# Optimization experiments

Hardware: AMD Instinct MI355X
Metric: run time of the kernel (lower is better)

Reference implementation:

```python
import jax, jax.numpy as jnp
import numpy as np

N = 512      # state dim n
K = 8        # num_regimes
H = 256      # hidden dim for g0/g1/gate MLPs
B = 8192     # batch
INIT_SCALE = 0.1


def _mlp(x, w1, b1, w2, b2, w3, b3):
    # 2 hidden SiLU layers + linear head (matches ScalarMLP/GateNet with num_layers=2)
    h = jax.nn.silu(x @ w1 + b1)
    h = jax.nn.silu(h @ w2 + b2)
    return h @ w3 + b3


def setup_inputs() -> dict:
    key = jax.random.key(0)
    ks = jax.random.split(key, 12)

    def lin(k, fi, fo):
        kw, kb = jax.random.split(k)
        s = 1.0 / np.sqrt(fi)  # torch nn.Linear default init range
        w = jax.random.uniform(kw, (fi, fo), minval=-s, maxval=s, dtype=jnp.float32)
        b = jax.random.uniform(kb, (fo,), minval=-s, maxval=s, dtype=jnp.float32)
        return w, b

    g0_w1, g0_b1 = lin(ks[0], N, H)
    g0_w2, g0_b2 = lin(ks[1], H, H)
    g0_w3, g0_b3 = lin(ks[2], H, 1)
    g1_w1, g1_b1 = lin(ks[3], N, H)
    g1_w2, g1_b2 = lin(ks[4], H, H)
    g1_w3, g1_b3 = lin(ks[5], H, 1)
    gt_w1, gt_b1 = lin(ks[6], N, H)
    gt_w2, gt_b2 = lin(ks[7], H, H)
    gt_w3, gt_b3 = lin(ks[8], H, K)
    W = jax.random.uniform(ks[9], (K, N, N), minval=-INIT_SCALE, maxval=INIT_SCALE, dtype=jnp.float32)
    z = jax.random.normal(ks[10], (B, 2 * N), dtype=jnp.float32)
    return dict(z=z,
                g0_w1=g0_w1, g0_b1=g0_b1, g0_w2=g0_w2, g0_b2=g0_b2, g0_w3=g0_w3, g0_b3=g0_b3,
                g1_w1=g1_w1, g1_b1=g1_b1, g1_w2=g1_w2, g1_b2=g1_b2, g1_w3=g1_w3, g1_b3=g1_b3,
                gt_w1=gt_w1, gt_b1=gt_b1, gt_w2=gt_w2, gt_b2=gt_b2, gt_w3=gt_w3, gt_b3=gt_b3,
                W=W)


def reference(z,
              g0_w1, g0_b1, g0_w2, g0_b2, g0_w3, g0_b3,
              g1_w1, g1_b1, g1_w2, g1_b2, g1_w3, g1_b3,
              gt_w1, gt_b1, gt_w2, gt_b2, gt_w3, gt_b3,
              W):
    n = W.shape[-1]
    x0, x1 = z[:, :n], z[:, n:]

    def U(x0_, x1_):
        e0 = jnp.sum(_mlp(x0_, g0_w1, g0_b1, g0_w2, g0_b2, g0_w3, g0_b3))  # scalar
        e1 = jnp.sum(_mlp(x1_, g1_w1, g1_b1, g1_w2, g1_b2, g1_w3, g1_b3))
        alpha = jax.nn.softmax(_mlp(x0_, gt_w1, gt_b1, gt_w2, gt_b2, gt_w3, gt_b3), axis=-1)  # [B,K]
        # per-sample per-regime bilinear x1^T W_k x0 -> avoids materializing [B,n,n] W_eff
        q = jnp.einsum('bi,kij,bj->bk', x1_, W, x0_)
        return e0 + e1 + jnp.sum(alpha * q)

    grad_x0, grad_x1 = jax.grad(U, argnums=(0, 1))(x0, x1)
    return jnp.concatenate([-grad_x0, -grad_x1], axis=-1)  # [B, 2n]
```

## Files before the change

kernel.cpp:

```cpp
#include <hip/hip_runtime.h>
#include <cstdint>
#include <cstddef>

constexpr int BTOT = 8192, N = 512, H = 256, K = 8;

typedef __attribute__((ext_vector_type(8))) short short8v;
typedef __attribute__((ext_vector_type(4))) float f32x4;

__device__ __forceinline__ float bf2f(unsigned short u) {
    return __uint_as_float(((uint32_t)u) << 16);
}
__device__ __forceinline__ unsigned short f2bf(float f) {
    uint32_t u = __float_as_uint(f);
    uint32_t r = (u + 0x7FFFu + ((u >> 16) & 1u)) >> 16;
    return (unsigned short)r;
}

typedef __attribute__((address_space(3))) unsigned int lds_uint;
typedef __attribute__((address_space(1))) const unsigned int glob_uint;
__device__ __forceinline__ void async16(const unsigned short* g, unsigned short* l) {
    __builtin_amdgcn_global_load_lds((glob_uint*)g, (lds_uint*)l, 16, 0, 0);
}

struct GArg {
    const unsigned short* A;
    const unsigned short* Bt;
    const float* bias;
    const unsigned short* dmul;
    const float* alpha;
    const unsigned short* vsub;
    unsigned short* ob;
    unsigned short* ob2;
    float* of;
    int lda, ldbt, Ka, lddm, ldob, ldof;
};

enum { EPI_BF = 0, EPI_FWD = 1, EPI_BWD2 = 2, EPI_NEG = 3, EPI_NEGV = 4 };

template<int EPI>
__global__ __launch_bounds__(256) void gemm_g(GArg ga0, GArg ga1, GArg ga2)
{
    const int z = blockIdx.z;
    const GArg g = (z == 0) ? ga0 : (z == 1) ? ga1 : ga2;

    __shared__ __attribute__((aligned(16))) unsigned short As[2][128 * 32];
    __shared__ __attribute__((aligned(16))) unsigned short Bs[2][128 * 32];
    const int tid = threadIdx.x;
    const int lane = tid & 63, wave = tid >> 6;
    const int m0 = blockIdx.y * 128, n0 = blockIdx.x * 128;
    const int wr = (wave >> 1) * 64, wc = (wave & 1) * 64;
    const int rr = lane & 15;
    const int kb = ((lane >> 4) ^ (lane & 3)) << 3;

    const int r0 = tid >> 2;
    const int ko0 = (((tid & 3) ^ (r0 & 3)) << 3);
    const unsigned short* gA0 = g.A + (size_t)(m0 + r0) * g.lda + ko0;
    const unsigned short* gA1 = g.A + (size_t)(m0 + r0 + 64) * g.lda + ko0;
    const unsigned short* gB0 = g.Bt + (size_t)(n0 + r0) * g.ldbt + ko0;
    const unsigned short* gB1 = g.Bt + (size_t)(n0 + r0 + 64) * g.ldbt + ko0;

    f32x4 acc[4][4];
    #pragma unroll
    for (int i = 0; i < 4; ++i)
        #pragma unroll
        for (int j = 0; j < 4; ++j) acc[i][j] = (f32x4){0.f, 0.f, 0.f, 0.f};

    const int nt = g.Ka >> 5;

    async16(gA0, &As[0][tid * 8]);
    async16(gA1, &As[0][(tid + 256) * 8]);
    async16(gB0, &Bs[0][tid * 8]);
    async16(gB1, &Bs[0][(tid + 256) * 8]);
    asm volatile("s_waitcnt vmcnt(0)" ::: "memory");
    __builtin_amdgcn_s_barrier();

    int cur = 0;
    for (int t = 0; t < nt; ++t) {
        if (t + 1 < nt) {
            const int k0 = (t + 1) << 5;
            async16(gA0 + k0, &As[cur ^ 1][tid * 8]);
            async16(gA1 + k0, &As[cur ^ 1][(tid + 256) * 8]);
            async16(gB0 + k0, &Bs[cur ^ 1][tid * 8]);
            async16(gB1 + k0, &Bs[cur ^ 1][(tid + 256) * 8]);
        }
        short8v af[4], bfr[4];
        #pragma unroll
        for (int i = 0; i < 4; ++i)
            af[i] = *(const short8v*)(&As[cur][(wr + i * 16 + rr) * 32 + kb]);
        #pragma unroll
        for (int j = 0; j < 4; ++j)
            bfr[j] = *(const short8v*)(&Bs[cur][(wc + j * 16 + rr) * 32 + kb]);
        #pragma unroll
        for (int i = 0; i < 4; ++i)
            #pragma unroll
            for (int j = 0; j < 4; ++j)
                acc[i][j] = __builtin_amdgcn_mfma_f32_16x16x32_bf16(af[i], bfr[j], acc[i][j], 0, 0, 0);
        asm volatile("s_waitcnt vmcnt(0)" ::: "memory");
        __builtin_amdgcn_s_barrier();
        cur ^= 1;
    }

    const int orow = (lane >> 4) * 4;
    #pragma unroll
    for (int i = 0; i < 4; ++i) {
        #pragma unroll
        for (int e = 0; e < 4; ++e) {
            const int row = m0 + wr + i * 16 + orow + e;
            if constexpr (EPI == EPI_NEGV) {
                float al[K];
                #pragma unroll
                for (int kk = 0; kk < K; ++kk) al[kk] = g.alpha[(size_t)row * K + kk];
                #pragma unroll
                for (int j = 0; j < 4; ++j) {
                    const int col = n0 + wc + rr + j * 16;
                    const unsigned short* vp = g.vsub + (size_t)row * (K * N) + col;
                    float sub = 0.f;
                    #pragma unroll
                    for (int kk = 0; kk < K; ++kk) sub += al[kk] * bf2f(vp[(size_t)kk * N]);
                    g.of[(size_t)row * g.ldof + col] = -acc[i][j][e] - sub;
                }
            } else {
                #pragma unroll
                for (int j = 0; j < 4; ++j) {
                    const int col = n0 + wc + rr + j * 16;
                    float v = acc[i][j][e];
                    if constexpr (EPI == EPI_BF) {
                        g.ob[(size_t)row * g.ldob + col] = f2bf(v);
                    } else if constexpr (EPI == EPI_FWD) {
                        float p = v + g.bias[col];
                        float s = 1.f / (1.f + expf(-p));
                        if (g.ob) g.ob[(size_t)row * g.ldob + col] = f2bf(p * s);
                        g.ob2[(size_t)row * g.ldob + col] = f2bf(s * (1.f + p * (1.f - s)));
                    } else if constexpr (EPI == EPI_BWD2) {
                        float t = v * bf2f(g.dmul[(size_t)row * g.lddm + col]);
                        g.ob[(size_t)row * g.ldob + col] = f2bf(t);
                    } else if constexpr (EPI == EPI_NEG) {
                        g.of[(size_t)row * g.ldof + col] -= v;
                    }
                }
            }
        }
    }
}

__global__ __launch_bounds__(256) void k_cvt_z(const float* __restrict__ z,
                                               unsigned short* __restrict__ o) {
    int g = (blockIdx.x * 256 + threadIdx.x) * 4;
    float4 v = *(const float4*)(z + g);
    ushort4 u;
    u.x = f2bf(v.x); u.y = f2bf(v.y); u.z = f2bf(v.z); u.w = f2bf(v.w);
    *(ushort4*)(o + g) = u;
}

__global__ __launch_bounds__(256) void k_transpose_w(const float* __restrict__ W,
    unsigned short* __restrict__ Wbf, unsigned short* __restrict__ WTbf)
{
    __shared__ float t[32][33];
    int k = blockIdx.z;
    int i0 = blockIdx.y * 32, j0 = blockIdx.x * 32;
    int tj = threadIdx.x & 31, ti = threadIdx.x >> 5;
    const float* Wk = W + (size_t)k * N * N;
    #pragma unroll
    for (int r = 0; r < 32; r += 8) {
        float v = Wk[(size_t)(i0 + ti + r) * N + j0 + tj];
        t[ti + r][tj] = v;
        Wbf[(size_t)k * N * N + (size_t)(i0 + ti + r) * N + j0 + tj] = f2bf(v);
    }
    __syncthreads();
    #pragma unroll
    for (int r = 0; r < 32; r += 8)
        WTbf[(size_t)k * N * N + (size_t)(j0 + ti + r) * N + i0 + tj] = f2bf(t[tj][ti + r]);
}

struct CvtJob { const float* src; unsigned short* dst; int ls, ld, cols32, tiles, trans; };
struct CvtTable { CvtJob j[12]; };

__global__ __launch_bounds__(256) void k_cvt_w(CvtTable T)
{
    int t = blockIdx.x;
    int ji = 0;
    while (t >= T.j[ji].tiles) { t -= T.j[ji].tiles; ++ji; }
    CvtJob jb = T.j[ji];
    int i0 = (t / jb.cols32) * 32, c0 = (t % jb.cols32) * 32;
    int tc = threadIdx.x & 31, tr = threadIdx.x >> 5;
    if (!jb.trans) {
        #pragma unroll
        for (int r = 0; r < 32; r += 8)
            jb.dst[(size_t)(i0 + tr + r) * jb.ld + c0 + tc] =
                f2bf(jb.src[(size_t)(i0 + tr + r) * jb.ls + c0 + tc]);
    } else {
        __shared__ float tt[32][33];
        #pragma unroll
        for (int r = 0; r < 32; r += 8)
            tt[tr + r][tc] = jb.src[(size_t)(i0 + tr + r) * jb.ls + c0 + tc];
        __syncthreads();
        #pragma unroll
        for (int r = 0; r < 32; r += 8)
            jb.dst[(size_t)(c0 + tr + r) * jb.ld + i0 + tc] = f2bf(tt[tc][tr + r]);
    }
}

__global__ __launch_bounds__(256) void k_head_s(const unsigned short* __restrict__ h2t,
    const float* __restrict__ w3t, const float* __restrict__ b3t,
    float* __restrict__ s)
{
    int t = threadIdx.x;
    int bl = t >> 3, k = t & 7;
    int b = blockIdx.x * 32 + bl;
    const unsigned short* ar = h2t + (size_t)b * H;
    float acc = b3t[k];
    for (int h0 = 0; h0 < H; h0 += 8) {
        short8v hv = *(const short8v*)(ar + h0);
        #pragma unroll
        for (int u = 0; u < 8; ++u)
            acc += bf2f((unsigned short)hv[u]) * w3t[(h0 + u) * K + k];
    }
    s[b * K + k] = acc;
}

__global__ __launch_bounds__(256) void k_q(const unsigned short* __restrict__ v0,
    const unsigned short* __restrict__ zb, float* __restrict__ q)
{
    int w = threadIdx.x >> 6, lane = threadIdx.x & 63;
    int idx = blockIdx.x * 4 + w;
    int b = idx >> 3, k = idx & 7;
    const unsigned short* vr = v0 + ((size_t)b * K + k) * N;
    const unsigned short* xr = zb + (size_t)b * 1024 + 512;
    short8v vv = *(const short8v*)(vr + lane * 8);
    short8v xv = *(const short8v*)(xr + lane * 8);
    float s = 0.f;
    #pragma unroll
    for (int t = 0; t < 8; ++t)
        s += bf2f((unsigned short)vv[t]) * bf2f((unsigned short)xv[t]);
    for (int off = 32; off; off >>= 1) s += __shfl_down(s, off, 64);
    if (lane == 0) q[idx] = s;
}

__global__ __launch_bounds__(256) void k_d(const float* __restrict__ s,
    const float* __restrict__ q, float* __restrict__ alpha,
    float* __restrict__ dd, int Bc)
{
    int b = blockIdx.x * 256 + threadIdx.x;
    if (b >= Bc) return;
    float sv[K], qv[K];
    float m = -1e30f;
    #pragma unroll
    for (int k = 0; k < K; ++k) { sv[k] = s[b * K + k]; m = fmaxf(m, sv[k]); }
    float sum = 0.f;
    #pragma unroll
    for (int k = 0; k < K; ++k) { sv[k] = expf(sv[k] - m); sum += sv[k]; }
    float inv = 1.f / sum, qbar = 0.f;
    #pragma unroll
    for (int k = 0; k < K; ++k) { sv[k] *= inv; qv[k] = q[b * K + k]; qbar += sv[k] * qv[k]; }
    #pragma unroll
    for (int k = 0; k < K; ++k) {
        alpha[b * K + k] = sv[k];
        dd[b * K + k] = sv[k] * (qv[k] - qbar);
    }
}

__global__ __launch_bounds__(256) void k_u2(
    const unsigned short* __restrict__ d2_0, const unsigned short* __restrict__ d2_1,
    const unsigned short* __restrict__ d2_t,
    const float* __restrict__ w3_0, const float* __restrict__ w3_1,
    const float* __restrict__ w3t, const float* __restrict__ dd,
    unsigned short* __restrict__ u2_0, unsigned short* __restrict__ u2_1,
    unsigned short* __restrict__ u2_t)
{
    int g = blockIdx.x * 256 + threadIdx.x;
    int h = g & (H - 1), b = g >> 8;
    u2_0[g] = f2bf(w3_0[h] * bf2f(d2_0[g]));
    u2_1[g] = f2bf(w3_1[h] * bf2f(d2_1[g]));
    float s = 0.f;
    #pragma unroll
    for (int k = 0; k < K; ++k) s += w3t[h * K + k] * dd[b * K + k];
    u2_t[g] = f2bf(s * bf2f(d2_t[g]));
}

__global__ __launch_bounds__(256) void k_gxq2(const unsigned short* __restrict__ v0,
    const unsigned short* __restrict__ v1, const float* __restrict__ alpha,
    float* __restrict__ out)
{
    int g = blockIdx.x * 256 + threadIdx.x;
    int b = g >> 6, jb = (g & 63) << 3;
    float al[K];
    #pragma unroll
    for (int k = 0; k < K; ++k) al[k] = alpha[b * K + k];
    const unsigned short* pv0 = v0 + (size_t)b * K * N + jb;
    const unsigned short* pv1 = v1 + (size_t)b * K * N + jb;
    float s0[8] = {}, s1[8] = {};
    #pragma unroll
    for (int k = 0; k < K; ++k) {
        short8v w1 = *(const short8v*)(pv1 + (size_t)k * N);
        short8v w0 = *(const short8v*)(pv0 + (size_t)k * N);
        #pragma unroll
        for (int t = 0; t < 8; ++t) {
            s0[t] += al[k] * bf2f((unsigned short)w1[t]);
            s1[t] += al[k] * bf2f((unsigned short)w0[t]);
        }
    }
    float* o0 = out + (size_t)b * 1024 + jb;
    float* o1 = o0 + 512;
    float4 x0 = *(float4*)o0, x1 = *(float4*)(o0 + 4);
    x0.x -= s0[0]; x0.y -= s0[1]; x0.z -= s0[2]; x0.w -= s0[3];
    x1.x -= s0[4]; x1.y -= s0[5]; x1.z -= s0[6]; x1.w -= s0[7];
    *(float4*)o0 = x0; *(float4*)(o0 + 4) = x1;
    float4 y0 = *(float4*)o1, y1 = *(float4*)(o1 + 4);
    y0.x -= s1[0]; y0.y -= s1[1]; y0.z -= s1[2]; y0.w -= s1[3];
    y1.x -= s1[4]; y1.y -= s1[5]; y1.z -= s1[6]; y1.w -= s1[7];
    *(float4*)o1 = y0; *(float4*)(o1 + 4) = y1;
}

extern "C" void kernel_launch(void* const* d_in, const int* in_sizes, int n_in,
                              void* d_out, int out_size, void* d_ws, size_t ws_size,
                              hipStream_t stream) {
    const float* z     = (const float*)d_in[0];
    const float* g0_w1 = (const float*)d_in[1];  const float* g0_b1 = (const float*)d_in[2];
    const float* g0_w2 = (const float*)d_in[3];  const float* g0_b2 = (const float*)d_in[4];
    const float* g0_w3 = (const float*)d_in[5];
    const float* g1_w1 = (const float*)d_in[7];  const float* g1_b1 = (const float*)d_in[8];
    const float* g1_w2 = (const float*)d_in[9];  const float* g1_b2 = (const float*)d_in[10];
    const float* g1_w3 = (const float*)d_in[11];
    const float* gt_w1 = (const float*)d_in[13]; const float* gt_b1 = (const float*)d_in[14];
    const float* gt_w2 = (const float*)d_in[15]; const float* gt_b2 = (const float*)d_in[16];
    const float* gt_w3 = (const float*)d_in[17]; const float* gt_b3 = (const float*)d_in[18];
    const float* W     = (const float*)d_in[19];
    float* out = (float*)d_out;

    char* wsb = (char*)d_ws;
    size_t off = 0;
    auto aus = [&](size_t n) -> unsigned short* {
        unsigned short* r = (unsigned short*)(wsb + off);
        off += ((n * 2 + 255) & ~(size_t)255);
        return r;
    };
    auto af4 = [&](size_t n) -> float* {
        float* r = (float*)(wsb + off);
        off += ((n * 4 + 255) & ~(size_t)255);
        return r;
    };

    unsigned short* Zbf  = aus((size_t)BTOT * 1024);
    unsigned short* Wbf  = aus((size_t)K * N * N);
    unsigned short* WTbf = aus((size_t)K * N * N);
    unsigned short* w1T[3], *w2T[3], *w2N[3];
    for (int i = 0; i < 3; ++i) w1T[i] = aus((size_t)H * N);
    for (int i = 0; i < 3; ++i) w2T[i] = aus((size_t)H * H);
    for (int i = 0; i < 3; ++i) w2N[i] = aus((size_t)H * H);
    unsigned short* w1N1  = aus((size_t)N * H);
    unsigned short* w1cat = aus((size_t)N * 2 * H);
    unsigned short* h1[3], *d1b[3], *d2b[3], *u2[3];
    for (int i = 0; i < 3; ++i) h1[i]  = aus((size_t)BTOT * H);
    for (int i = 0; i < 3; ++i) d1b[i] = aus((size_t)BTOT * H);
    for (int i = 0; i < 3; ++i) d2b[i] = aus((size_t)BTOT * H);
    for (int i = 0; i < 3; ++i) u2[i]  = aus((size_t)BTOT * H);
    unsigned short* h2t   = aus((size_t)BTOT * H);
    unsigned short* t2cat = aus((size_t)BTOT * 512);
    unsigned short* t21   = aus((size_t)BTOT * H);
    float* sbuf = af4((size_t)BTOT * K);
    float* qbuf = af4((size_t)BTOT * K);
    float* abuf = af4((size_t)BTOT * K);
    float* dbuf = af4((size_t)BTOT * K);

    int Bcv = BTOT;
    while (off + 2 * (((size_t)Bcv * K * N * 2 + 255) & ~(size_t)255) > ws_size && Bcv > 128)
        Bcv >>= 1;
    unsigned short* v0 = aus((size_t)Bcv * K * N);
    unsigned short* v1 = aus((size_t)Bcv * K * N);
    const bool full = (Bcv == BTOT);

    const dim3 blk(256);

    if (!full)
        hipMemsetAsync(d_out, 0, (size_t)out_size * sizeof(float), stream);

    k_cvt_z<<<BTOT * 1024 / (256 * 4), blk, 0, stream>>>(z, Zbf);
    k_transpose_w<<<dim3(N / 32, N / 32, K), blk, 0, stream>>>(W, Wbf, WTbf);

    CvtTable T;
    int nj = 0, tot = 0;
    auto addjob = [&](const float* src, int ls, unsigned short* dst, int ld,
                      int rows, int cols, int trans) {
        CvtJob jb; jb.src = src; jb.dst = dst; jb.ls = ls; jb.ld = ld;
        jb.cols32 = cols / 32; jb.tiles = (rows / 32) * (cols / 32); jb.trans = trans;
        T.j[nj++] = jb; tot += jb.tiles;
    };
    addjob(g0_w1, H, w1T[0], N, N, H, 1);
    addjob(g1_w1, H, w1T[1], N, N, H, 1);
    addjob(gt_w1, H, w1T[2], N, N, H, 1);
    addjob(g0_w2, H, w2T[0], H, H, H, 1);
    addjob(g1_w2, H, w2T[1], H, H, H, 1);
    addjob(gt_w2, H, w2T[2], H, H, H, 1);
    addjob(g0_w2, H, w2N[0], H, H, H, 0);
    addjob(g1_w2, H, w2N[1], H, H, H, 0);
    addjob(gt_w2, H, w2N[2], H, H, H, 0);
    addjob(g1_w1, H, w1N1, H, N, H, 0);
    addjob(g0_w1, H, w1cat, 2 * H, N, H, 0);
    addjob(gt_w1, H, w1cat + H, 2 * H, N, H, 0);
    k_cvt_w<<<tot, blk, 0, stream>>>(T);

    auto mk = [](const unsigned short* A, int lda, const unsigned short* Bt, int ldbt, int Ka) {
        GArg g; g.A = A; g.Bt = Bt; g.bias = nullptr; g.dmul = nullptr;
        g.alpha = nullptr; g.vsub = nullptr;
        g.ob = nullptr; g.ob2 = nullptr; g.of = nullptr;
        g.lda = lda; g.ldbt = ldbt; g.Ka = Ka; g.lddm = 0; g.ldob = 0; g.ldof = 0;
        return g;
    };

    {
        const float* bs[3] = {g0_b1, g1_b1, gt_b1};
        GArg a[3];
        for (int i = 0; i < 3; ++i) {
            a[i] = mk(Zbf + (i == 1 ? 512 : 0), 1024, w1T[i], N, N);
            a[i].bias = bs[i]; a[i].ob = h1[i]; a[i].ob2 = d1b[i]; a[i].ldob = H;
        }
        gemm_g<EPI_FWD><<<dim3(H / 128, BTOT / 128, 3), blk, 0, stream>>>(a[0], a[1], a[2]);
    }
    {
        const float* bs[3] = {g0_b2, g1_b2, gt_b2};
        GArg a[3];
        for (int i = 0; i < 3; ++i) {
            a[i] = mk(h1[i], H, w2T[i], H, H);
            a[i].bias = bs[i]; a[i].ob = (i == 2) ? h2t : nullptr;
            a[i].ob2 = d2b[i]; a[i].ldob = H;
        }
        gemm_g<EPI_FWD><<<dim3(H / 128, BTOT / 128, 3), blk, 0, stream>>>(a[0], a[1], a[2]);
    }
    k_head_s<<<BTOT / 32, blk, 0, stream>>>(h2t, gt_w3, gt_b3, sbuf);

    for (int cb = 0; cb < BTOT; cb += Bcv) {
        GArg a[2];
        a[0] = mk(Zbf + (size_t)cb * 1024, 1024, Wbf, N, N);
        a[0].ob = v0; a[0].ldob = K * N;
        a[1] = mk(Zbf + (size_t)cb * 1024 + 512, 1024, WTbf, N, N);
        a[1].ob = v1; a[1].ldob = K * N;
        gemm_g<EPI_BF><<<dim3(K * N / 128, Bcv / 128, 2), blk, 0, stream>>>(a[0], a[1], a[1]);

        k_q<<<Bcv * K / 4, blk, 0, stream>>>(v0, Zbf + (size_t)cb * 1024, qbuf + (size_t)cb * K);
        k_d<<<(Bcv + 255) / 256, blk, 0, stream>>>(sbuf + (size_t)cb * K, qbuf + (size_t)cb * K,
                                                   abuf + (size_t)cb * K, dbuf + (size_t)cb * K, Bcv);
        if (!full)
            k_gxq2<<<Bcv * 64 / 256, blk, 0, stream>>>(v0, v1, abuf + (size_t)cb * K,
                                                       out + (size_t)cb * 1024);
    }

    k_u2<<<BTOT * H / 256, blk, 0, stream>>>(d2b[0], d2b[1], d2b[2],
                                             g0_w3, g1_w3, gt_w3, dbuf,
                                             u2[0], u2[1], u2[2]);

    {
        GArg a[3];
        a[0] = mk(u2[0], H, w2N[0], H, H);
        a[0].dmul = d1b[0]; a[0].lddm = H; a[0].ob = t2cat;     a[0].ldob = 512;
        a[1] = mk(u2[1], H, w2N[1], H, H);
        a[1].dmul = d1b[1]; a[1].lddm = H; a[1].ob = t21;       a[1].ldob = H;
        a[2] = mk(u2[2], H, w2N[2], H, H);
        a[2].dmul = d1b[2]; a[2].lddm = H; a[2].ob = t2cat + H; a[2].ldob = 512;
        gemm_g<EPI_BWD2><<<dim3(H / 128, BTOT / 128, 3), blk, 0, stream>>>(a[0], a[1], a[2]);
    }
    {
        GArg a[2];
        a[0] = mk(t2cat, 512, w1cat, 2 * H, 512);
        a[0].of = out;       a[0].ldof = 1024;
        a[1] = mk(t21, H, w1N1, H, H);
        a[1].of = out + 512; a[1].ldof = 1024;
        if (full) {
            a[0].alpha = abuf; a[0].vsub = v1;
            a[1].alpha = abuf; a[1].vsub = v0;
            gemm_g<EPI_NEGV><<<dim3(N / 128, BTOT / 128, 2), blk, 0, stream>>>(a[0], a[1], a[1]);
        } else {
            gemm_g<EPI_NEG><<<dim3(N / 128, BTOT / 128, 2), blk, 0, stream>>>(a[0], a[1], a[1]);
        }
    }
}
```

Before: 247.4 us.

## Fuse gate head and bilinear q reductions into GEMM epilogues via atomics

The gate head logits (h2·w3) are now reduced inside the second-layer forward GEMM epilogue, and q = x1·v0 inside the v0/v1 GEMM epilogue. Both use cross-lane shuffles plus atomicAdd into pre-zeroed buffers, which removes the k_head_s and k_q kernels and the h2t write and re-read. The gate bias is added later in k_d. A block-index swizzle over the N dimension is also added to change tile scheduling order. The costs are extra epilogue work, two memsets, atomic contention, and float atomics whose summation order is nondeterministic.

```diff
diff --git a/kernel.cpp b/kernel.cpp
--- a/kernel.cpp
+++ b/kernel.cpp
@@ -32,6 +32,10 @@
     unsigned short* ob;
     unsigned short* ob2;
     float* of;
+    float* qout;
+    const unsigned short* xq;
+    float* sout;
+    const float* w3s;
     int lda, ldbt, Ka, lddm, ldob, ldof;
 };
 
@@ -47,7 +51,11 @@
     __shared__ __attribute__((aligned(16))) unsigned short Bs[2][128 * 32];
     const int tid = threadIdx.x;
     const int lane = tid & 63, wave = tid >> 6;
-    const int m0 = blockIdx.y * 128, n0 = blockIdx.x * 128;
+
+    int bx = blockIdx.x;
+    if ((gridDim.x & 7) == 0) bx = (bx & 7) * (gridDim.x >> 3) + (bx >> 3);
+
+    const int m0 = blockIdx.y * 128, n0 = bx * 128;
     const int wr = (wave >> 1) * 64, wc = (wave & 1) * 64;
     const int rr = lane & 15;
     const int kb = ((lane >> 4) ^ (lane & 3)) << 3;
@@ -119,6 +127,38 @@
                     for (int kk = 0; kk < K; ++kk) sub += al[kk] * bf2f(vp[(size_t)kk * N]);
                     g.of[(size_t)row * g.ldof + col] = -acc[i][j][e] - sub;
                 }
+            } else if constexpr (EPI == EPI_FWD) {
+                float sq[K];
+                const bool do_s = (g.sout != nullptr);
+                #pragma unroll
+                for (int kk = 0; kk < K; ++kk) sq[kk] = 0.f;
+                #pragma unroll
+                for (int j = 0; j < 4; ++j) {
+                    const int col = n0 + wc + rr + j * 16;
+                    float p = acc[i][j][e] + g.bias[col];
+                    float s = 1.f / (1.f + expf(-p));
+                    if (g.ob) g.ob[(size_t)row * g.ldob + col] = f2bf(p * s);
+                    g.ob2[(size_t)row * g.ldob + col] = f2bf(s * (1.f + p * (1.f - s)));
+                    if (do_s) {
+                        float sl = p * s;
+                        float4 wa = *(const float4*)(g.w3s + (size_t)col * K);
+                        float4 wb = *(const float4*)(g.w3s + (size_t)col * K + 4);
+                        sq[0] += sl * wa.x; sq[1] += sl * wa.y;
+                        sq[2] += sl * wa.z; sq[3] += sl * wa.w;
+                        sq[4] += sl * wb.x; sq[5] += sl * wb.y;
+                        sq[6] += sl * wb.z; sq[7] += sl * wb.w;
+                    }
+                }
+                if (do_s) {
+                    #pragma unroll
+                    for (int m = 1; m < 16; m <<= 1)
+                        #pragma unroll
+                        for (int kk = 0; kk < K; ++kk) sq[kk] += __shfl_xor(sq[kk], m, 64);
+                    if ((lane & 15) == 0)
+                        #pragma unroll
+                        for (int kk = 0; kk < K; ++kk)
+                            atomicAdd(g.sout + (size_t)row * K + kk, sq[kk]);
+                }
             } else {
                 #pragma unroll
                 for (int j = 0; j < 4; ++j) {
@@ -126,11 +166,6 @@
                     float v = acc[i][j][e];
                     if constexpr (EPI == EPI_BF) {
                         g.ob[(size_t)row * g.ldob + col] = f2bf(v);
-                    } else if constexpr (EPI == EPI_FWD) {
-                        float p = v + g.bias[col];
-                        float s = 1.f / (1.f + expf(-p));
-                        if (g.ob) g.ob[(size_t)row * g.ldob + col] = f2bf(p * s);
-                        g.ob2[(size_t)row * g.ldob + col] = f2bf(s * (1.f + p * (1.f - s)));
                     } else if constexpr (EPI == EPI_BWD2) {
                         float t = v * bf2f(g.dmul[(size_t)row * g.lddm + col]);
                         g.ob[(size_t)row * g.ldob + col] = f2bf(t);
@@ -139,6 +174,21 @@
                     }
                 }
             }
+            if constexpr (EPI == EPI_BF) {
+                if (g.qout) {
+                    const int kq = n0 >> 9, i0 = n0 & 511;
+                    float sqv = 0.f;
+                    #pragma unroll
+                    for (int j = 0; j < 4; ++j) {
+                        const int ic = i0 + wc + rr + j * 16;
+                        sqv += acc[i][j][e] * bf2f(g.xq[(size_t)row * 1024 + ic]);
+                    }
+                    #pragma unroll
+                    for (int m = 1; m < 16; m <<= 1) sqv += __shfl_xor(sqv, m, 64);
+                    if ((lane & 15) == 0)
+                        atomicAdd(g.qout + (size_t)row * K + kq, sqv);
+                }
+            }
         }
     }
 }
@@ -200,43 +250,8 @@
     }
 }
 
-__global__ __launch_bounds__(256) void k_head_s(const unsigned short* __restrict__ h2t,
-    const float* __restrict__ w3t, const float* __restrict__ b3t,
-    float* __restrict__ s)
-{
-    int t = threadIdx.x;
-    int bl = t >> 3, k = t & 7;
-    int b = blockIdx.x * 32 + bl;
-    const unsigned short* ar = h2t + (size_t)b * H;
-    float acc = b3t[k];
-    for (int h0 = 0; h0 < H; h0 += 8) {
-        short8v hv = *(const short8v*)(ar + h0);
-        #pragma unroll
-        for (int u = 0; u < 8; ++u)
-            acc += bf2f((unsigned short)hv[u]) * w3t[(h0 + u) * K + k];
-    }
-    s[b * K + k] = acc;
-}
-
-__global__ __launch_bounds__(256) void k_q(const unsigned short* __restrict__ v0,
-    const unsigned short* __restrict__ zb, float* __restrict__ q)
-{
-    int w = threadIdx.x >> 6, lane = threadIdx.x & 63;
-    int idx = blockIdx.x * 4 + w;
-    int b = idx >> 3, k = idx & 7;
-    const unsigned short* vr = v0 + ((size_t)b * K + k) * N;
-    const unsigned short* xr = zb + (size_t)b * 1024 + 512;
-    short8v vv = *(const short8v*)(vr + lane * 8);
-    short8v xv = *(const short8v*)(xr + lane * 8);
-    float s = 0.f;
-    #pragma unroll
-    for (int t = 0; t < 8; ++t)
-        s += bf2f((unsigned short)vv[t]) * bf2f((unsigned short)xv[t]);
-    for (int off = 32; off; off >>= 1) s += __shfl_down(s, off, 64);
-    if (lane == 0) q[idx] = s;
-}
-
 __global__ __launch_bounds__(256) void k_d(const float* __restrict__ s,
+    const float* __restrict__ b3t,
     const float* __restrict__ q, float* __restrict__ alpha,
     float* __restrict__ dd, int Bc)
 {
@@ -245,7 +260,7 @@
     float sv[K], qv[K];
     float m = -1e30f;
     #pragma unroll
-    for (int k = 0; k < K; ++k) { sv[k] = s[b * K + k]; m = fmaxf(m, sv[k]); }
+    for (int k = 0; k < K; ++k) { sv[k] = s[b * K + k] + b3t[k]; m = fmaxf(m, sv[k]); }
     float sum = 0.f;
     #pragma unroll
     for (int k = 0; k < K; ++k) { sv[k] = expf(sv[k] - m); sum += sv[k]; }
@@ -354,7 +369,6 @@
     for (int i = 0; i < 3; ++i) d1b[i] = aus((size_t)BTOT * H);
     for (int i = 0; i < 3; ++i) d2b[i] = aus((size_t)BTOT * H);
     for (int i = 0; i < 3; ++i) u2[i]  = aus((size_t)BTOT * H);
-    unsigned short* h2t   = aus((size_t)BTOT * H);
     unsigned short* t2cat = aus((size_t)BTOT * 512);
     unsigned short* t21   = aus((size_t)BTOT * H);
     float* sbuf = af4((size_t)BTOT * K);
@@ -373,6 +387,8 @@
 
     if (!full)
         hipMemsetAsync(d_out, 0, (size_t)out_size * sizeof(float), stream);
+    hipMemsetAsync(qbuf, 0, (size_t)BTOT * K * sizeof(float), stream);
+    hipMemsetAsync(sbuf, 0, (size_t)BTOT * K * sizeof(float), stream);
 
     k_cvt_z<<<BTOT * 1024 / (256 * 4), blk, 0, stream>>>(z, Zbf);
     k_transpose_w<<<dim3(N / 32, N / 32, K), blk, 0, stream>>>(W, Wbf, WTbf);
@@ -403,6 +419,7 @@
         GArg g; g.A = A; g.Bt = Bt; g.bias = nullptr; g.dmul = nullptr;
         g.alpha = nullptr; g.vsub = nullptr;
         g.ob = nullptr; g.ob2 = nullptr; g.of = nullptr;
+        g.qout = nullptr; g.xq = nullptr; g.sout = nullptr; g.w3s = nullptr;
         g.lda = lda; g.ldbt = ldbt; g.Ka = Ka; g.lddm = 0; g.ldob = 0; g.ldof = 0;
         return g;
     };
@@ -421,23 +438,25 @@
         GArg a[3];
         for (int i = 0; i < 3; ++i) {
             a[i] = mk(h1[i], H, w2T[i], H, H);
-            a[i].bias = bs[i]; a[i].ob = (i == 2) ? h2t : nullptr;
+            a[i].bias = bs[i]; a[i].ob = nullptr;
             a[i].ob2 = d2b[i]; a[i].ldob = H;
         }
+        a[2].sout = sbuf; a[2].w3s = gt_w3;
         gemm_g<EPI_FWD><<<dim3(H / 128, BTOT / 128, 3), blk, 0, stream>>>(a[0], a[1], a[2]);
     }
-    k_head_s<<<BTOT / 32, blk, 0, stream>>>(h2t, gt_w3, gt_b3, sbuf);
 
     for (int cb = 0; cb < BTOT; cb += Bcv) {
         GArg a[2];
         a[0] = mk(Zbf + (size_t)cb * 1024, 1024, Wbf, N, N);
         a[0].ob = v0; a[0].ldob = K * N;
+        a[0].qout = qbuf + (size_t)cb * K;
+        a[0].xq = Zbf + (size_t)cb * 1024 + 512;
         a[1] = mk(Zbf + (size_t)cb * 1024 + 512, 1024, WTbf, N, N);
         a[1].ob = v1; a[1].ldob = K * N;
         gemm_g<EPI_BF><<<dim3(K * N / 128, Bcv / 128, 2), blk, 0, stream>>>(a[0], a[1], a[1]);
 
-        k_q<<<Bcv * K / 4, blk, 0, stream>>>(v0, Zbf + (size_t)cb * 1024, qbuf + (size_t)cb * K);
-        k_d<<<(Bcv + 255) / 256, blk, 0, stream>>>(sbuf + (size_t)cb * K, qbuf + (size_t)cb * K,
+        k_d<<<(Bcv + 255) / 256, blk, 0, stream>>>(sbuf + (size_t)cb * K, gt_b3,
+                                                   qbuf + (size_t)cb * K,
                                                    abuf + (size_t)cb * K, dbuf + (size_t)cb * K, Bcv);
         if (!full)
             k_gxq2<<<Bcv * 64 / 256, blk, 0, stream>>>(v0, v1, abuf + (size_t)cb * K,
```

New measurement: 309.1 us. +24.9%, slower.

## Triple-buffer GEMM LDS tiles with two-stage-ahead async prefetch

Applied to the files above, without the earlier changes.

The bf16 MFMA GEMM moves from double to triple buffering of the A/B LDS tiles and issues async global-to-LDS loads two K-steps ahead. A partial vmcnt wait lets the next tile's loads stay in flight while the current tile is consumed, and one barrier per iteration replaces the full drain at the end of each step. The cost is 50% more LDS per block, which may reduce occupancy.

```diff
diff --git a/kernel.cpp b/kernel.cpp
--- a/kernel.cpp
+++ b/kernel.cpp
@@ -43,8 +43,8 @@
     const int z = blockIdx.z;
     const GArg g = (z == 0) ? ga0 : (z == 1) ? ga1 : ga2;
 
-    __shared__ __attribute__((aligned(16))) unsigned short As[2][128 * 32];
-    __shared__ __attribute__((aligned(16))) unsigned short Bs[2][128 * 32];
+    __shared__ __attribute__((aligned(16))) unsigned short As[3][128 * 32];
+    __shared__ __attribute__((aligned(16))) unsigned short Bs[3][128 * 32];
     const int tid = threadIdx.x;
     const int lane = tid & 63, wave = tid >> 6;
     const int m0 = blockIdx.y * 128, n0 = blockIdx.x * 128;
@@ -59,6 +59,14 @@
     const unsigned short* gB0 = g.Bt + (size_t)(n0 + r0) * g.ldbt + ko0;
     const unsigned short* gB1 = g.Bt + (size_t)(n0 + r0 + 64) * g.ldbt + ko0;
 
+    auto stage = [&](int t, int buf) {
+        const int k0 = t << 5;
+        async16(gA0 + k0, &As[buf][tid * 8]);
+        async16(gA1 + k0, &As[buf][(tid + 256) * 8]);
+        async16(gB0 + k0, &Bs[buf][tid * 8]);
+        async16(gB1 + k0, &Bs[buf][(tid + 256) * 8]);
+    };
+
     f32x4 acc[4][4];
     #pragma unroll
     for (int i = 0; i < 4; ++i)
@@ -67,37 +75,31 @@
 
     const int nt = g.Ka >> 5;
 
-    async16(gA0, &As[0][tid * 8]);
-    async16(gA1, &As[0][(tid + 256) * 8]);
-    async16(gB0, &Bs[0][tid * 8]);
-    async16(gB1, &Bs[0][(tid + 256) * 8]);
-    asm volatile("s_waitcnt vmcnt(0)" ::: "memory");
-    __builtin_amdgcn_s_barrier();
-
-    int cur = 0;
+    stage(0, 0);
+    if (nt > 1) stage(1, 1);
+
+    int buf = 0;
     for (int t = 0; t < nt; ++t) {
-        if (t + 1 < nt) {
-            const int k0 = (t + 1) << 5;
-            async16(gA0 + k0, &As[cur ^ 1][tid * 8]);
-            async16(gA1 + k0, &As[cur ^ 1][(tid + 256) * 8]);
-            async16(gB0 + k0, &Bs[cur ^ 1][tid * 8]);
-            async16(gB1 + k0, &Bs[cur ^ 1][(tid + 256) * 8]);
+        if (t + 1 < nt) { asm volatile("s_waitcnt vmcnt(4)" ::: "memory"); }
+        else            { asm volatile("s_waitcnt vmcnt(0)" ::: "memory"); }
+        __builtin_amdgcn_s_barrier();
+        if (t + 2 < nt) {
+            int b2 = buf + 2; if (b2 >= 3) b2 -= 3;
+            stage(t + 2, b2);
         }
         short8v af[4], bfr[4];
         #pragma unroll
         for (int i = 0; i < 4; ++i)
-            af[i] = *(const short8v*)(&As[cur][(wr + i * 16 + rr) * 32 + kb]);
+            af[i] = *(const short8v*)(&As[buf][(wr + i * 16 + rr) * 32 + kb]);
         #pragma unroll
         for (int j = 0; j < 4; ++j)
-            bfr[j] = *(const short8v*)(&Bs[cur][(wc + j * 16 + rr) * 32 + kb]);
+            bfr[j] = *(const short8v*)(&Bs[buf][(wc + j * 16 + rr) * 32 + kb]);
         #pragma unroll
         for (int i = 0; i < 4; ++i)
             #pragma unroll
             for (int j = 0; j < 4; ++j)
                 acc[i][j] = __builtin_amdgcn_mfma_f32_16x16x32_bf16(af[i], bfr[j], acc[i][j], 0, 0, 0);
-        asm volatile("s_waitcnt vmcnt(0)" ::: "memory");
-        __builtin_amdgcn_s_barrier();
-        cur ^= 1;
+        if (++buf == 3) buf = 0;
     }
 
     const int orow = (lane >> 4) * 4;
```

New measurement: 246.1 us, median of 2. About the same (-0.5%).
